# Optimization experiments

Measured on AMD Instinct MI355X. Metric: run time of the kernel, lower is better.

Reference implementation:

```python
import jax, jax.numpy as jnp
import numpy as np

# ---- constants (from init_kwargs / Box defaults) ----
B, K, T = 32768, 256, 10
C_LIGHT, F0, DF = 3.0e8, 1.0e10, 3.0e4
D_EL = C_LIGHT / (2.0 * F0)            # half-wavelength spacing
SPATIAL = F0 * D_EL / C_LIGHT          # = 0.5
RANGE_C = 2.0 * DF / C_LIGHT           # = 2e-4
THETA_MIN, THETA_MAX = -60.0, 60.0
R_MIN, R_MAX = 0.0, 2000.0
BETA = 2.0
STEP_CLIP = 0.1
INIT_ALPHA, INIT_LAMBDA = 0.01, 0.001
ALPHA_MIN, ALPHA_MAX = 1e-6, 0.2
LAM_MIN, LAM_MAX = 1e-6, 1.0
EPS = 1e-6


def _atanh(y):
    return jnp.arctanh(jnp.clip(y, -1.0 + EPS, 1.0 - EPS))


def map_theta_r_to_u(theta_deg, r_m):
    mid = 0.5 * (THETA_MIN + THETA_MAX)
    half = 0.5 * (THETA_MAX - THETA_MIN)
    y = (theta_deg - mid) / half
    s = jnp.clip((r_m - R_MIN) / (R_MAX - R_MIN), EPS, 1.0 - EPS)
    u_r = _atanh(2.0 * s - 1.0)          # tanh r_box inverse
    return jnp.stack([_atanh(y), u_r], axis=-1)  # (B,2)


def map_u_to_theta_r(u):
    mid = 0.5 * (THETA_MIN + THETA_MAX)
    half = 0.5 * (THETA_MAX - THETA_MIN)
    theta = mid + half * jnp.tanh(u[:, 0])
    s = 0.5 * (jnp.tanh(u[:, 1]) + 1.0)
    r = R_MIN + (R_MAX - R_MIN) * s
    return theta, r


def steering(theta_deg, r_m):
    # FDA steering: phase_k = 2*pi*k*(0.5*sin(theta) - 2*df*r/c)
    k = jnp.arange(K, dtype=jnp.float32)
    th = theta_deg * (jnp.pi / 180.0)
    phase = (2.0 * jnp.pi) * k[None, :] * (
        SPATIAL * jnp.sin(th)[:, None] - RANGE_C * r_m[:, None])  # (B,K)
    inv_sqrt_k = 1.0 / np.sqrt(K)
    return jnp.cos(phase) * inv_sqrt_k, jnp.sin(phase) * inv_sqrt_k


def loglike_logistic(theta_deg, r_m, z_re, z_im):
    # 1-bit logistic log-likelihood, summed over array elements -> (B,)
    a_re, a_im = steering(theta_deg, r_m)
    ll = jax.nn.log_sigmoid(BETA * z_re * a_re) + jax.nn.log_sigmoid(BETA * z_im * a_im)
    return jnp.sum(ll, axis=-1)


def setup_inputs() -> dict:
    key = jax.random.key(0)
    k1, k2, k3, k4 = jax.random.split(key, 4)
    z_real = jnp.sign(jax.random.normal(k1, (B, K), dtype=jnp.float32))
    z_imag = jnp.sign(jax.random.normal(k2, (B, K), dtype=jnp.float32))
    theta0 = jax.random.uniform(k3, (B,), jnp.float32, -55.0, 55.0)
    r0 = jax.random.uniform(k4, (B,), jnp.float32, 100.0, 1900.0)
    a_raw0 = float(np.log(np.expm1(INIT_ALPHA)))   # inverse softplus
    l_raw0 = float(np.log(np.expm1(INIT_LAMBDA)))
    return {
        "z_real": z_real, "z_imag": z_imag,
        "theta0_deg": theta0, "r0_m": r0,
        "alpha_theta_raw": jnp.full((T,), a_raw0, jnp.float32),
        "alpha_r_raw": jnp.full((T,), a_raw0, jnp.float32),
        "lambda_theta_raw": jnp.full((T,), l_raw0, jnp.float32),
        "lambda_r_raw": jnp.full((T,), l_raw0, jnp.float32),
    }


def reference(z_real, z_imag, theta0_deg, r0_m,
              alpha_theta_raw, alpha_r_raw, lambda_theta_raw, lambda_r_raw):
    alpha_th = jnp.clip(jax.nn.softplus(alpha_theta_raw), ALPHA_MIN, ALPHA_MAX)
    alpha_r = jnp.clip(jax.nn.softplus(alpha_r_raw), ALPHA_MIN, ALPHA_MAX)
    lam_th = jnp.clip(jax.nn.softplus(lambda_theta_raw), LAM_MIN, LAM_MAX)
    lam_r = jnp.clip(jax.nn.softplus(lambda_r_raw), LAM_MIN, LAM_MAX)

    u0 = map_theta_r_to_u(theta0_deg, r0_m)  # (B,2)

    def neg_obj_sum(u):
        th, r = map_u_to_theta_r(u)
        return -jnp.sum(loglike_logistic(th, r, z_real, z_imag))

    grad_fn = jax.grad(neg_obj_sum)

    def body(u, params):
        a_th, a_r, l_th, l_r = params
        # first-order unroll: gradient is a constant w.r.t. outer autodiff
        g = jax.lax.stop_gradient(grad_fn(u))
        g = jnp.where(jnp.isfinite(g), g, 0.0)
        g_th, g_r = g[:, 0], g[:, 1]
        a_th = jnp.where(jnp.isfinite(a_th), a_th, INIT_ALPHA)
        a_r = jnp.where(jnp.isfinite(a_r), a_r, INIT_ALPHA)
        l_th = jnp.where(jnp.isfinite(l_th), l_th, INIT_LAMBDA)
        l_r = jnp.where(jnp.isfinite(l_r), l_r, INIT_LAMBDA)
        den_th = jnp.maximum(jnp.nan_to_num(
            jnp.maximum(jnp.abs(g_th), 1e-6) + l_th, nan=1.0, posinf=1.0, neginf=1.0), 1e-6)
        den_r = jnp.maximum(jnp.nan_to_num(
            jnp.maximum(jnp.abs(g_r), 1e-6) + l_r, nan=1.0, posinf=1.0, neginf=1.0), 1e-6)
        step_u = jnp.stack([a_th * g_th / den_th, a_r * g_r / den_r], axis=-1)
        step_u = jnp.clip(jnp.nan_to_num(step_u, nan=0.0, posinf=0.0, neginf=0.0),
                          -STEP_CLIP, STEP_CLIP)
        return u - step_u, None

    uT, _ = jax.lax.scan(body, u0, (alpha_th, alpha_r, lam_th, lam_r))
    theta_T, r_T = map_u_to_theta_r(uT)
    return jnp.stack([theta_T, r_T], axis=-1)  # (B,2)
```

## Files before the change

### kernel.cpp

```cpp
#include <hip/hip_runtime.h>
#include <cstdint>

#define PI_F 3.14159265358979323846f

typedef float v2f __attribute__((ext_vector_type(2)));

__device__ __forceinline__ float fract_(float x)  { return __builtin_amdgcn_fractf(x); }
__device__ __forceinline__ float sin2pi_(float r) { return __builtin_amdgcn_sinf(r); }
__device__ __forceinline__ float cos2pi_(float r) { return __builtin_amdgcn_cosf(r); }
__device__ __forceinline__ v2f  splat2(float x)   { v2f r; r.x = x; r.y = x; return r; }

extern "C" __global__ void __launch_bounds__(256)
pack_signs(const float4* __restrict__ zr, const float4* __restrict__ zi,
           uint32_t* __restrict__ pr, uint32_t* __restrict__ pim) {
    const int t = blockIdx.x * 256 + threadIdx.x;
    uint32_t wr = 0u, wi = 0u;
    #pragma unroll
    for (int q = 0; q < 8; ++q) {
        const float4 a = zr[t * 8 + q];
        const float4 b = zi[t * 8 + q];
        wr |= ((uint32_t)(a.x < 0.f) << (4 * q))     | ((uint32_t)(a.y < 0.f) << (4 * q + 1))
            | ((uint32_t)(a.z < 0.f) << (4 * q + 2)) | ((uint32_t)(a.w < 0.f) << (4 * q + 3));
        wi |= ((uint32_t)(b.x < 0.f) << (4 * q))     | ((uint32_t)(b.y < 0.f) << (4 * q + 1))
            | ((uint32_t)(b.z < 0.f) << (4 * q + 2)) | ((uint32_t)(b.w < 0.f) << (4 * q + 3));
    }
    pr[t] = wr;
    pim[t] = wi;
}

extern "C" __global__ void __launch_bounds__(256)
refine(const float* __restrict__ th0, const float* __restrict__ r0,
       const float* __restrict__ a_th_raw, const float* __restrict__ a_r_raw,
       const float* __restrict__ l_th_raw, const float* __restrict__ l_r_raw,
       const uint32_t* __restrict__ pr, const uint32_t* __restrict__ pim,
       float* __restrict__ out) {
    const int lane = threadIdx.x & 63;
    const int w    = threadIdx.x >> 6;
    const int item = blockIdx.x * 64 + lane;

    __shared__ float sp[4][10];
    __shared__ float red[2][4][64];

    if (threadIdx.x < 40) {
        const int a = threadIdx.x / 10, i = threadIdx.x % 10;
        const float* src = (a == 0) ? a_th_raw : (a == 1) ? a_r_raw
                         : (a == 2) ? l_th_raw : l_r_raw;
        const float v  = log1pf(expf(src[i]));
        const float hi = (a < 2) ? 0.2f : 1.0f;
        sp[a][i] = fminf(fmaxf(v, 1e-6f), hi);
    }

    const uint32_t br0 = pr [item * 8 + w * 2 + 0];
    const uint32_t br1 = pr [item * 8 + w * 2 + 1];
    const uint32_t bi0 = pim[item * 8 + w * 2 + 0];
    const uint32_t bi1 = pim[item * 8 + w * 2 + 1];

    float y = th0[item] * (1.0f / 60.0f);
    y = fminf(fmaxf(y, -1.0f + 1e-6f), 1.0f - 1e-6f);
    float u0 = atanhf(y);
    float sR = r0[item] * (1.0f / 2000.0f);
    sR = fminf(fmaxf(sR, 1e-6f), 1.0f - 1e-6f);
    float u1 = atanhf(2.0f * sR - 1.0f);

    const float w64 = (float)(w * 64);

    __syncthreads();

    for (int t = 0; t < 10; ++t) {
        const float ath = sp[0][t], ar = sp[1][t], lth = sp[2][t], lr = sp[3][t];

        const float T0 = tanhf(u0), T1 = tanhf(u1);
        const float th_rad = (PI_F / 3.0f) * T0;
        const float sth = sinf(th_rad), cth = cosf(th_rad);
        const float r   = 1000.0f * (T1 + 1.0f);
        const float crev = 0.5f * sth - 2e-4f * r;

        const float d4 = fract_(4.0f * crev);
        const v2f C4 = splat2(cos2pi_(d4));
        const v2f S4 = splat2(sin2pi_(d4));

        v2f c[2], s[2], kf[2], acc[2];
        #pragma unroll
        for (int p2 = 0; p2 < 2; ++p2) {
            const float k0a = w64 + (float)(2 * p2);
            const float k0b = w64 + (float)(2 * p2 + 1);
            const float rva = fract_(k0a * crev);
            const float rvb = fract_(k0b * crev);
            v2f cc, ssv, kk;
            cc.x  = cos2pi_(rva);  cc.y  = cos2pi_(rvb);
            ssv.x = sin2pi_(rva);  ssv.y = sin2pi_(rvb);
            kk.x  = k0a;           kk.y  = k0b;
            c[p2]   = cc;
            s[p2]   = ssv;
            kf[p2]  = kk;
            acc[p2] = splat2(0.0f);
        }

        const v2f mtwo = splat2(-2.0f);
        const v2f one  = splat2(1.0f);
        const v2f cub  = splat2(-(1.0f / 196608.0f));
        const v2f four = splat2(4.0f);

        #pragma unroll
        for (int j = 0; j < 16; ++j) {
            #pragma unroll
            for (int p2 = 0; p2 < 2; ++p2) {
                const int klA = 2 * p2 + 4 * j;
                const int klB = klA + 1;
                const uint32_t wr = (klA < 32) ? br0 : br1;
                const uint32_t wi = (klA < 32) ? bi0 : bi1;
                const uint32_t mreA = (wr << (31 - (klA & 31))) & 0x80000000u;
                const uint32_t mreB = (wr << (31 - (klB & 31))) & 0x80000000u;
                const uint32_t mimA = (wi << (31 - (klA & 31))) & 0x80000000u;
                const uint32_t mimB = (wi << (31 - (klB & 31))) & 0x80000000u;
                const v2f cs = c[p2], ss = s[p2];
                v2f zc, zs;
                zc.x = __uint_as_float(__float_as_uint(cs.x) ^ mimA);
                zc.y = __uint_as_float(__float_as_uint(cs.y) ^ mimB);
                zs.x = __uint_as_float(__float_as_uint(ss.x) ^ mreA);
                zs.y = __uint_as_float(__float_as_uint(ss.y) ^ mreB);
                const v2f w0 = zc - zs;
                const v2f u2 = ss * ss;
                const v2f t2 = __builtin_elementwise_fma(mtwo, u2, one);
                const v2f sc = ss * cs;
                const v2f v  = sc * t2;
                const v2f W  = __builtin_elementwise_fma(v, cub, w0 * 0.0625f);
                acc[p2] = __builtin_elementwise_fma(kf[p2], W, acc[p2]);
                kf[p2]  = kf[p2] + four;
                const v2f tA = ss * S4;
                const v2f tB = cs * S4;
                c[p2] = __builtin_elementwise_fma(cs, C4, -tA);
                s[p2] = __builtin_elementwise_fma(ss, C4, tB);
            }
        }
        float S = (acc[0].x + acc[0].y) + (acc[1].x + acc[1].y);

        const int p = t & 1;
        red[p][w][lane] = S;
        __syncthreads();
        S = (red[p][0][lane] + red[p][1][lane]) + (red[p][2][lane] + red[p][3][lane]);

        const float g0 = -(PI_F * PI_F / 3.0f) * cth * (1.0f - T0 * T0) * S;
        const float g1 = 0.4f * PI_F * (1.0f - T1 * T1) * S;
        const float den0 = fmaxf(fabsf(g0), 1e-6f) + lth;
        const float den1 = fmaxf(fabsf(g1), 1e-6f) + lr;
        float st0 = ath * g0 / den0;
        float st1 = ar  * g1 / den1;
        st0 = fminf(fmaxf(st0, -0.1f), 0.1f);
        st1 = fminf(fmaxf(st1, -0.1f), 0.1f);
        u0 -= st0;
        u1 -= st1;
    }

    if (w == 0) {
        const float thT = 60.0f * tanhf(u0);
        const float rT  = 1000.0f * (tanhf(u1) + 1.0f);
        reinterpret_cast<float2*>(out)[item] = make_float2(thT, rT);
    }
}

extern "C" void kernel_launch(void* const* d_in, const int* in_sizes, int n_in,
                              void* d_out, int out_size, void* d_ws, size_t ws_size,
                              hipStream_t stream) {
    const float* zr   = (const float*)d_in[0];
    const float* zi   = (const float*)d_in[1];
    const float* th0  = (const float*)d_in[2];
    const float* r0   = (const float*)d_in[3];
    const float* athr = (const float*)d_in[4];
    const float* arr  = (const float*)d_in[5];
    const float* lthr = (const float*)d_in[6];
    const float* lrr  = (const float*)d_in[7];

    const int B  = in_sizes[2];
    const int BK = in_sizes[0];

    uint32_t* pr  = (uint32_t*)d_ws;
    uint32_t* pim = pr + (size_t)B * 8;

    pack_signs<<<(BK / 32) / 256, 256, 0, stream>>>((const float4*)zr, (const float4*)zi,
                                                    pr, pim);
    refine<<<B / 64, 256, 0, stream>>>(th0, r0, athr, arr, lthr, lrr, pr, pim,
                                       (float*)d_out);
}
```

Before: 139.2 us.

## Fuse sign packing into refine kernel and reduce K-chunks with wave shuffles

Drops the separate pack_signs kernel. The refine kernel now reads the float z inputs directly and builds its sign bitmasks in registers. Threads are remapped so the four K-chunks of one batch item sit in the same wavefront (16 items per wave). That lets the per-iteration partial-sum reduction use two xor shuffles instead of an LDS buffer and a __syncthreads. This removes one kernel launch, the workspace round trip and ten block barriers. The cost is strided float4 loads, 1 KB apart per item, which may coalesce less well than the old packing kernel.

```diff
diff --git a/kernel.cpp b/kernel.cpp
--- a/kernel.cpp
+++ b/kernel.cpp
@@ -11,35 +11,18 @@
 __device__ __forceinline__ v2f  splat2(float x)   { v2f r; r.x = x; r.y = x; return r; }
 
 extern "C" __global__ void __launch_bounds__(256)
-pack_signs(const float4* __restrict__ zr, const float4* __restrict__ zi,
-           uint32_t* __restrict__ pr, uint32_t* __restrict__ pim) {
-    const int t = blockIdx.x * 256 + threadIdx.x;
-    uint32_t wr = 0u, wi = 0u;
-    #pragma unroll
-    for (int q = 0; q < 8; ++q) {
-        const float4 a = zr[t * 8 + q];
-        const float4 b = zi[t * 8 + q];
-        wr |= ((uint32_t)(a.x < 0.f) << (4 * q))     | ((uint32_t)(a.y < 0.f) << (4 * q + 1))
-            | ((uint32_t)(a.z < 0.f) << (4 * q + 2)) | ((uint32_t)(a.w < 0.f) << (4 * q + 3));
-        wi |= ((uint32_t)(b.x < 0.f) << (4 * q))     | ((uint32_t)(b.y < 0.f) << (4 * q + 1))
-            | ((uint32_t)(b.z < 0.f) << (4 * q + 2)) | ((uint32_t)(b.w < 0.f) << (4 * q + 3));
-    }
-    pr[t] = wr;
-    pim[t] = wi;
-}
-
-extern "C" __global__ void __launch_bounds__(256)
 refine(const float* __restrict__ th0, const float* __restrict__ r0,
        const float* __restrict__ a_th_raw, const float* __restrict__ a_r_raw,
        const float* __restrict__ l_th_raw, const float* __restrict__ l_r_raw,
-       const uint32_t* __restrict__ pr, const uint32_t* __restrict__ pim,
+       const float4* __restrict__ zr4, const float4* __restrict__ zi4,
        float* __restrict__ out) {
     const int lane = threadIdx.x & 63;
     const int w    = threadIdx.x >> 6;
-    const int item = blockIdx.x * 64 + lane;
+    const int il   = lane & 15;
+    const int cw   = lane >> 4;
+    const int item = blockIdx.x * 64 + w * 16 + il;
 
     __shared__ float sp[4][10];
-    __shared__ float red[2][4][64];
 
     if (threadIdx.x < 40) {
         const int a = threadIdx.x / 10, i = threadIdx.x % 10;
@@ -50,10 +33,24 @@
         sp[a][i] = fminf(fmaxf(v, 1e-6f), hi);
     }
 
-    const uint32_t br0 = pr [item * 8 + w * 2 + 0];
-    const uint32_t br1 = pr [item * 8 + w * 2 + 1];
-    const uint32_t bi0 = pim[item * 8 + w * 2 + 0];
-    const uint32_t bi1 = pim[item * 8 + w * 2 + 1];
+    const float4* za = zr4 + (size_t)item * 64 + (size_t)cw * 16;
+    const float4* zb = zi4 + (size_t)item * 64 + (size_t)cw * 16;
+    uint32_t br0 = 0u, br1 = 0u, bi0 = 0u, bi1 = 0u;
+    #pragma unroll
+    for (int q = 0; q < 8; ++q) {
+        const float4 a0 = za[q];
+        const float4 a1 = za[q + 8];
+        const float4 b0 = zb[q];
+        const float4 b1 = zb[q + 8];
+        br0 |= ((uint32_t)(a0.x < 0.f) << (4 * q))     | ((uint32_t)(a0.y < 0.f) << (4 * q + 1))
+             | ((uint32_t)(a0.z < 0.f) << (4 * q + 2)) | ((uint32_t)(a0.w < 0.f) << (4 * q + 3));
+        br1 |= ((uint32_t)(a1.x < 0.f) << (4 * q))     | ((uint32_t)(a1.y < 0.f) << (4 * q + 1))
+             | ((uint32_t)(a1.z < 0.f) << (4 * q + 2)) | ((uint32_t)(a1.w < 0.f) << (4 * q + 3));
+        bi0 |= ((uint32_t)(b0.x < 0.f) << (4 * q))     | ((uint32_t)(b0.y < 0.f) << (4 * q + 1))
+             | ((uint32_t)(b0.z < 0.f) << (4 * q + 2)) | ((uint32_t)(b0.w < 0.f) << (4 * q + 3));
+        bi1 |= ((uint32_t)(b1.x < 0.f) << (4 * q))     | ((uint32_t)(b1.y < 0.f) << (4 * q + 1))
+             | ((uint32_t)(b1.z < 0.f) << (4 * q + 2)) | ((uint32_t)(b1.w < 0.f) << (4 * q + 3));
+    }
 
     float y = th0[item] * (1.0f / 60.0f);
     y = fminf(fmaxf(y, -1.0f + 1e-6f), 1.0f - 1e-6f);
@@ -62,7 +59,7 @@
     sR = fminf(fmaxf(sR, 1e-6f), 1.0f - 1e-6f);
     float u1 = atanhf(2.0f * sR - 1.0f);
 
-    const float w64 = (float)(w * 64);
+    const float w64 = (float)(cw * 64);
 
     __syncthreads();
 
@@ -135,10 +132,8 @@
         }
         float S = (acc[0].x + acc[0].y) + (acc[1].x + acc[1].y);
 
-        const int p = t & 1;
-        red[p][w][lane] = S;
-        __syncthreads();
-        S = (red[p][0][lane] + red[p][1][lane]) + (red[p][2][lane] + red[p][3][lane]);
+        S += __shfl_xor(S, 16, 64);
+        S += __shfl_xor(S, 32, 64);
 
         const float g0 = -(PI_F * PI_F / 3.0f) * cth * (1.0f - T0 * T0) * S;
         const float g1 = 0.4f * PI_F * (1.0f - T1 * T1) * S;
@@ -152,7 +147,7 @@
         u1 -= st1;
     }
 
-    if (w == 0) {
+    if (cw == 0) {
         const float thT = 60.0f * tanhf(u0);
         const float rT  = 1000.0f * (tanhf(u1) + 1.0f);
         reinterpret_cast<float2*>(out)[item] = make_float2(thT, rT);
@@ -171,14 +166,9 @@
     const float* lthr = (const float*)d_in[6];
     const float* lrr  = (const float*)d_in[7];
 
-    const int B  = in_sizes[2];
-    const int BK = in_sizes[0];
+    const int B = in_sizes[2];
 
-    uint32_t* pr  = (uint32_t*)d_ws;
-    uint32_t* pim = pr + (size_t)B * 8;
-
-    pack_signs<<<(BK / 32) / 256, 256, 0, stream>>>((const float4*)zr, (const float4*)zi,
-                                                    pr, pim);
-    refine<<<B / 64, 256, 0, stream>>>(th0, r0, athr, arr, lthr, lrr, pr, pim,
+    refine<<<B / 64, 256, 0, stream>>>(th0, r0, athr, arr, lthr, lrr,
+                                       (const float4*)zr, (const float4*)zi,
                                        (float*)d_out);
 }
```

Result: slower. 149.9 us (+7.7%).
